# Kernel optimization log

Measured on AMD Instinct MI355X. Metric: run time of the kernel, lower is better.

Reference implementation:

```python
import jax, jax.numpy as jnp
import numpy as np

N, IN_DIM, OUT_DIM = 8192, 256, 128
NEG_BIG = -9e15


def setup_inputs() -> dict:
    key = jax.random.key(0)
    k_x, k_a, k_w, k_att = jax.random.split(key, 4)
    X = jax.random.normal(k_x, (N, IN_DIM), dtype=jnp.float32)
    A = jax.random.randint(k_a, (N, N), 0, 2).astype(jnp.float32)
    # nn.Linear(in_dim, out_dim, bias=False): weight [out_dim, in_dim]
    W = jax.random.normal(k_w, (OUT_DIM, IN_DIM), dtype=jnp.float32) / np.sqrt(IN_DIM)
    # nn.Linear(out_dim, 1, bias=False): weight [1, out_dim] -> store as [out_dim]
    a_w = jax.random.normal(k_att, (OUT_DIM,), dtype=jnp.float32) / np.sqrt(OUT_DIM)
    return {"X": X, "A": A, "W": W, "a_w": a_w}


def reference(X, A, W, a_w):
    Wh = X @ W.T                                  # [N, out_dim]
    e = jax.nn.relu(Wh) @ a_w                      # [N]  (a(relu(Wh)).squeeze(-1))
    # NOTE: faithful to source: e broadcasts over rows -> score[i, j] = e[j]
    scores = jnp.where(A > 0, e[None, :], NEG_BIG)  # [N, N]
    attention = jax.nn.softmax(scores, axis=1)      # [N, N]
    h_prime = attention @ Wh                        # [N, out_dim]
    return jax.nn.relu(h_prime)
```

## Files before the change

### kernel.cpp

```cpp
#include <hip/hip_runtime.h>

typedef float        f32x4  __attribute__((ext_vector_type(4)));
typedef __bf16       bf16x8 __attribute__((ext_vector_type(8)));
typedef unsigned int u32x4  __attribute__((ext_vector_type(4)));

#define NN   8192
#define IND  256
#define OUTD 128
#define NB   144
#define KSPLIT 8
#define KRANGE 1024
#define KCHUNK 128
#define BSTRIDE 136

__device__ __forceinline__ bf16x8 cvt2(f32x4 a, f32x4 b) {
  bf16x8 r;
  r[0]=(__bf16)a[0]; r[1]=(__bf16)a[1]; r[2]=(__bf16)a[2]; r[3]=(__bf16)a[3];
  r[4]=(__bf16)b[0]; r[5]=(__bf16)b[1]; r[6]=(__bf16)b[2]; r[7]=(__bf16)b[3];
  return r;
}

__global__ __launch_bounds__(128) void k1_wh_e(const float* __restrict__ X,
                                               const float* __restrict__ W,
                                               const float* __restrict__ aw,
                                               float* __restrict__ Wh,
                                               float* __restrict__ ev) {
  const int lane = threadIdx.x & 63;
  const int wave = threadIdx.x >> 6;
  const int nlo  = lane & 15;
  const int quad = lane >> 4;
  const int rowBase = blockIdx.x * 32 + wave * 16;

  const float* xp = X + (size_t)(rowBase + nlo) * IND + quad * 8;
  f32x4 acc[8];
#pragma unroll
  for (int nt = 0; nt < 8; ++nt) acc[nt] = f32x4{0.f, 0.f, 0.f, 0.f};

#pragma unroll
  for (int kb = 0; kb < IND; kb += 32) {
    f32x4 a0 = *(const f32x4*)(xp + kb);
    f32x4 a1 = *(const f32x4*)(xp + kb + 4);
    bf16x8 af = cvt2(a0, a1);
#pragma unroll
    for (int nt = 0; nt < 8; ++nt) {
      const float* wp = W + (size_t)(nt * 16 + nlo) * IND + kb + quad * 8;
      f32x4 b0 = *(const f32x4*)wp;
      f32x4 b1 = *(const f32x4*)(wp + 4);
      acc[nt] = __builtin_amdgcn_mfma_f32_16x16x32_bf16(af, cvt2(b0, b1), acc[nt], 0, 0, 0);
    }
  }
  float p0 = 0.f, p1 = 0.f, p2 = 0.f, p3 = 0.f;
#pragma unroll
  for (int nt = 0; nt < 8; ++nt) {
    const int col = nt * 16 + nlo;
    const float awc = aw[col];
    const int r0 = rowBase + quad * 4;
    float v0 = acc[nt][0], v1 = acc[nt][1], v2 = acc[nt][2], v3 = acc[nt][3];
    Wh[(size_t)(r0 + 0) * OUTD + col] = v0;
    Wh[(size_t)(r0 + 1) * OUTD + col] = v1;
    Wh[(size_t)(r0 + 2) * OUTD + col] = v2;
    Wh[(size_t)(r0 + 3) * OUTD + col] = v3;
    p0 += fmaxf(v0, 0.f) * awc;
    p1 += fmaxf(v1, 0.f) * awc;
    p2 += fmaxf(v2, 0.f) * awc;
    p3 += fmaxf(v3, 0.f) * awc;
  }
#pragma unroll
  for (int off = 8; off; off >>= 1) {
    p0 += __shfl_xor(p0, off, 64);
    p1 += __shfl_xor(p1, off, 64);
    p2 += __shfl_xor(p2, off, 64);
    p3 += __shfl_xor(p3, off, 64);
  }
  if (nlo == 0) {
    const int r0 = rowBase + quad * 4;
    ev[r0 + 0] = p0; ev[r0 + 1] = p1; ev[r0 + 2] = p2; ev[r0 + 3] = p3;
  }
}

__global__ __launch_bounds__(256) void k2_bt(const float* __restrict__ Wh,
                                             const float* __restrict__ ev,
                                             __bf16* __restrict__ Bt) {
  const int j = blockIdx.x * 256 + threadIdx.x;
  const float w = expf(ev[j]);
  const int n0 = blockIdx.y * 18;
#pragma unroll
  for (int i = 0; i < 18; ++i) {
    const int n = n0 + i;
    float v = 0.f;
    if (n < OUTD) v = w * Wh[(size_t)j * OUTD + n];
    else if (n == OUTD) v = w;
    Bt[(size_t)n * NN + j] = (__bf16)v;
  }
}

__global__ __launch_bounds__(256, 4) void k3_partial(const float* __restrict__ Adj,
                                                     const __bf16* __restrict__ Bt,
                                                     float* __restrict__ part) {
  __shared__ unsigned short bt[NB * BSTRIDE];
  const int tid  = threadIdx.x;
  const int lane = tid & 63;
  const int wave = tid >> 6;
  const int nlo  = lane & 15;
  const int quad = lane >> 4;
  const int rowW = blockIdx.x * 64 + wave * 16;
  const int k0   = blockIdx.y * KRANGE;

  const int brow = tid >> 4;
  const int bcol = (tid & 15) * 8;

  f32x4 acc[9];
#pragma unroll
  for (int nt = 0; nt < 9; ++nt) acc[nt] = f32x4{0.f, 0.f, 0.f, 0.f};

  const float* ap = Adj + (size_t)(rowW + nlo) * NN + quad * 8 + k0;

  for (int c = 0; c < KRANGE / KCHUNK; ++c) {
    const int kc = k0 + c * KCHUNK;
    u32x4 breg[9];
#pragma unroll
    for (int rr = 0; rr < 9; ++rr)
      breg[rr] = *(const u32x4*)(Bt + (size_t)(rr * 16 + brow) * NN + kc + bcol);
    f32x4 areg[8];
#pragma unroll
    for (int s = 0; s < 4; ++s) {
      areg[2 * s]     = __builtin_nontemporal_load((const f32x4*)(ap + c * KCHUNK + s * 32));
      areg[2 * s + 1] = __builtin_nontemporal_load((const f32x4*)(ap + c * KCHUNK + s * 32 + 4));
    }
#pragma unroll
    for (int rr = 0; rr < 9; ++rr)
      *(u32x4*)(bt + (rr * 16 + brow) * BSTRIDE + bcol) = breg[rr];
    __syncthreads();
#pragma unroll
    for (int s = 0; s < 4; ++s) {
      bf16x8 af = cvt2(areg[2 * s], areg[2 * s + 1]);
      const unsigned short* bp = bt + s * 32 + quad * 8;
#pragma unroll
      for (int nt = 0; nt < 9; ++nt) {
        bf16x8 bf = *(const bf16x8*)(bp + (nt * 16 + nlo) * BSTRIDE);
        acc[nt] = __builtin_amdgcn_mfma_f32_16x16x32_bf16(af, bf, acc[nt], 0, 0, 0);
      }
    }
    __syncthreads();
  }

  float* pbase = part + ((size_t)blockIdx.y * NN + rowW) * NB;
#pragma unroll
  for (int nt = 0; nt < 9; ++nt)
#pragma unroll
    for (int rg = 0; rg < 4; ++rg)
      pbase[(size_t)(quad * 4 + rg) * NB + nt * 16 + nlo] = acc[nt][rg];
}

__global__ __launch_bounds__(256) void k3_reduce(const float* __restrict__ part,
                                                 float* __restrict__ out) {
  const int col = threadIdx.x & 127;
  const int row = blockIdx.x * 2 + (threadIdx.x >> 7);
  float num = 0.f, den = 0.f;
#pragma unroll
  for (int s = 0; s < KSPLIT; ++s) {
    const size_t base = ((size_t)s * NN + row) * NB;
    num += part[base + col];
    den += part[base + 128];
  }
  out[(size_t)row * OUTD + col] = fmaxf(num / den, 0.f);
}

extern "C" void kernel_launch(void* const* d_in, const int* in_sizes, int n_in,
                              void* d_out, int out_size, void* d_ws, size_t ws_size,
                              hipStream_t stream) {
  const float* X  = (const float*)d_in[0];
  const float* A  = (const float*)d_in[1];
  const float* W  = (const float*)d_in[2];
  const float* aw = (const float*)d_in[3];
  float* out = (float*)d_out;

  char* ws = (char*)d_ws;
  float*  Wh   = (float*)ws;
  float*  ev   = (float*)(ws + 4194304);
  __bf16* Bt   = (__bf16*)(ws + 4227072);
  float*  part = (float*)(ws + 8388608);

  k1_wh_e<<<256, 128, 0, stream>>>(X, W, aw, Wh, ev);
  k2_bt<<<dim3(32, 8), 256, 0, stream>>>(Wh, ev, Bt);
  k3_partial<<<dim3(128, KSPLIT), 256, 0, stream>>>(A, Bt, part);
  k3_reduce<<<4096, 256, 0, stream>>>(part, out);
}
```

Before: 432.2 us.

## Fuse Bt construction into Wh kernel and read B operand directly from global

The first kernel now computes exp(e), scales Wh in registers and writes the transposed bf16 B matrix, including the denominator row and zero padding, directly. This removes the intermediate fp32 Wh/ev round trip and one kernel launch. The main attention kernel drops its LDS staging of B and the two barriers per chunk, loading B fragments straight from global memory and relying on L2/L1 reuse across blocks. The cost is possibly less coalesced B loads per wave and more cache traffic in the bandwidth-bound stage that streams A.

```diff
diff --git a/kernel.cpp b/kernel.cpp
--- a/kernel.cpp
+++ b/kernel.cpp
@@ -2,7 +2,7 @@
 
 typedef float        f32x4  __attribute__((ext_vector_type(4)));
 typedef __bf16       bf16x8 __attribute__((ext_vector_type(8)));
-typedef unsigned int u32x4  __attribute__((ext_vector_type(4)));
+typedef __bf16       bf16x4 __attribute__((ext_vector_type(4)));
 
 #define NN   8192
 #define IND  256
@@ -11,7 +11,6 @@
 #define KSPLIT 8
 #define KRANGE 1024
 #define KCHUNK 128
-#define BSTRIDE 136
 
 __device__ __forceinline__ bf16x8 cvt2(f32x4 a, f32x4 b) {
   bf16x8 r;
@@ -20,11 +19,10 @@
   return r;
 }
 
-__global__ __launch_bounds__(128) void k1_wh_e(const float* __restrict__ X,
-                                               const float* __restrict__ W,
-                                               const float* __restrict__ aw,
-                                               float* __restrict__ Wh,
-                                               float* __restrict__ ev) {
+__global__ __launch_bounds__(128) void k1_bt(const float* __restrict__ X,
+                                             const float* __restrict__ W,
+                                             const float* __restrict__ aw,
+                                             __bf16* __restrict__ Bt) {
   const int lane = threadIdx.x & 63;
   const int wave = threadIdx.x >> 6;
   const int nlo  = lane & 15;
@@ -49,21 +47,15 @@
       acc[nt] = __builtin_amdgcn_mfma_f32_16x16x32_bf16(af, cvt2(b0, b1), acc[nt], 0, 0, 0);
     }
   }
+
   float p0 = 0.f, p1 = 0.f, p2 = 0.f, p3 = 0.f;
 #pragma unroll
   for (int nt = 0; nt < 8; ++nt) {
-    const int col = nt * 16 + nlo;
-    const float awc = aw[col];
-    const int r0 = rowBase + quad * 4;
-    float v0 = acc[nt][0], v1 = acc[nt][1], v2 = acc[nt][2], v3 = acc[nt][3];
-    Wh[(size_t)(r0 + 0) * OUTD + col] = v0;
-    Wh[(size_t)(r0 + 1) * OUTD + col] = v1;
-    Wh[(size_t)(r0 + 2) * OUTD + col] = v2;
-    Wh[(size_t)(r0 + 3) * OUTD + col] = v3;
-    p0 += fmaxf(v0, 0.f) * awc;
-    p1 += fmaxf(v1, 0.f) * awc;
-    p2 += fmaxf(v2, 0.f) * awc;
-    p3 += fmaxf(v3, 0.f) * awc;
+    const float awc = aw[nt * 16 + nlo];
+    p0 += fmaxf(acc[nt][0], 0.f) * awc;
+    p1 += fmaxf(acc[nt][1], 0.f) * awc;
+    p2 += fmaxf(acc[nt][2], 0.f) * awc;
+    p3 += fmaxf(acc[nt][3], 0.f) * awc;
   }
 #pragma unroll
   for (int off = 8; off; off >>= 1) {
@@ -72,55 +64,53 @@
     p2 += __shfl_xor(p2, off, 64);
     p3 += __shfl_xor(p3, off, 64);
   }
+  const float w0 = expf(p0), w1 = expf(p1), w2 = expf(p2), w3 = expf(p3);
+  const int r0 = rowBase + quad * 4;
+
+#pragma unroll
+  for (int nt = 0; nt < 8; ++nt) {
+    bf16x4 o;
+    o[0] = (__bf16)(acc[nt][0] * w0);
+    o[1] = (__bf16)(acc[nt][1] * w1);
+    o[2] = (__bf16)(acc[nt][2] * w2);
+    o[3] = (__bf16)(acc[nt][3] * w3);
+    *(bf16x4*)(Bt + (size_t)(nt * 16 + nlo) * NN + r0) = o;
+  }
   if (nlo == 0) {
-    const int r0 = rowBase + quad * 4;
-    ev[r0 + 0] = p0; ev[r0 + 1] = p1; ev[r0 + 2] = p2; ev[r0 + 3] = p3;
+    bf16x4 ow;
+    ow[0] = (__bf16)w0; ow[1] = (__bf16)w1; ow[2] = (__bf16)w2; ow[3] = (__bf16)w3;
+    *(bf16x4*)(Bt + (size_t)OUTD * NN + r0) = ow;
   }
-}
-
-__global__ __launch_bounds__(256) void k2_bt(const float* __restrict__ Wh,
-                                             const float* __restrict__ ev,
-                                             __bf16* __restrict__ Bt) {
-  const int j = blockIdx.x * 256 + threadIdx.x;
-  const float w = expf(ev[j]);
-  const int n0 = blockIdx.y * 18;
-#pragma unroll
-  for (int i = 0; i < 18; ++i) {
-    const int n = n0 + i;
-    float v = 0.f;
-    if (n < OUTD) v = w * Wh[(size_t)j * OUTD + n];
-    else if (n == OUTD) v = w;
-    Bt[(size_t)n * NN + j] = (__bf16)v;
+  {
+    const int t = threadIdx.x;
+    if (t < 120) {
+      const int row = 129 + (t >> 3);
+      const int cg  = (t & 7) * 4;
+      bf16x4 z;
+      z[0] = (__bf16)0.f; z[1] = (__bf16)0.f; z[2] = (__bf16)0.f; z[3] = (__bf16)0.f;
+      *(bf16x4*)(Bt + (size_t)row * NN + blockIdx.x * 32 + cg) = z;
+    }
   }
 }
 
 __global__ __launch_bounds__(256, 4) void k3_partial(const float* __restrict__ Adj,
                                                      const __bf16* __restrict__ Bt,
                                                      float* __restrict__ part) {
-  __shared__ unsigned short bt[NB * BSTRIDE];
-  const int tid  = threadIdx.x;
-  const int lane = tid & 63;
-  const int wave = tid >> 6;
+  const int lane = threadIdx.x & 63;
+  const int wave = threadIdx.x >> 6;
   const int nlo  = lane & 15;
   const int quad = lane >> 4;
   const int rowW = blockIdx.x * 64 + wave * 16;
   const int k0   = blockIdx.y * KRANGE;
 
-  const int brow = tid >> 4;
-  const int bcol = (tid & 15) * 8;
-
   f32x4 acc[9];
 #pragma unroll
   for (int nt = 0; nt < 9; ++nt) acc[nt] = f32x4{0.f, 0.f, 0.f, 0.f};
 
-  const float* ap = Adj + (size_t)(rowW + nlo) * NN + quad * 8 + k0;
+  const float*  ap = Adj + (size_t)(rowW + nlo) * NN + quad * 8 + k0;
+  const __bf16* bp = Bt  + (size_t)nlo * NN + quad * 8 + k0;
 
   for (int c = 0; c < KRANGE / KCHUNK; ++c) {
-    const int kc = k0 + c * KCHUNK;
-    u32x4 breg[9];
-#pragma unroll
-    for (int rr = 0; rr < 9; ++rr)
-      breg[rr] = *(const u32x4*)(Bt + (size_t)(rr * 16 + brow) * NN + kc + bcol);
     f32x4 areg[8];
 #pragma unroll
     for (int s = 0; s < 4; ++s) {
@@ -128,20 +118,14 @@
       areg[2 * s + 1] = __builtin_nontemporal_load((const f32x4*)(ap + c * KCHUNK + s * 32 + 4));
     }
 #pragma unroll
-    for (int rr = 0; rr < 9; ++rr)
-      *(u32x4*)(bt + (rr * 16 + brow) * BSTRIDE + bcol) = breg[rr];
-    __syncthreads();
-#pragma unroll
     for (int s = 0; s < 4; ++s) {
       bf16x8 af = cvt2(areg[2 * s], areg[2 * s + 1]);
-      const unsigned short* bp = bt + s * 32 + quad * 8;
 #pragma unroll
       for (int nt = 0; nt < 9; ++nt) {
-        bf16x8 bf = *(const bf16x8*)(bp + (nt * 16 + nlo) * BSTRIDE);
+        bf16x8 bf = *(const bf16x8*)(bp + (size_t)(nt * 16) * NN + c * KCHUNK + s * 32);
         acc[nt] = __builtin_amdgcn_mfma_f32_16x16x32_bf16(af, bf, acc[nt], 0, 0, 0);
       }
     }
-    __syncthreads();
   }
 
   float* pbase = part + ((size_t)blockIdx.y * NN + rowW) * NB;
@@ -176,13 +160,10 @@
   float* out = (float*)d_out;
 
   char* ws = (char*)d_ws;
-  float*  Wh   = (float*)ws;
-  float*  ev   = (float*)(ws + 4194304);
-  __bf16* Bt   = (__bf16*)(ws + 4227072);
-  float*  part = (float*)(ws + 8388608);
+  __bf16* Bt   = (__bf16*)ws;
+  float*  part = (float*)(ws + 4194304);
 
-  k1_wh_e<<<256, 128, 0, stream>>>(X, W, aw, Wh, ev);
-  k2_bt<<<dim3(32, 8), 256, 0, stream>>>(Wh, ev, Bt);
+  k1_bt<<<256, 128, 0, stream>>>(X, W, aw, Bt);
   k3_partial<<<dim3(128, KSPLIT), 256, 0, stream>>>(A, Bt, part);
   k3_reduce<<<4096, 256, 0, stream>>>(part, out);
 }
```

Measured after the change: 500.5 us. +15.8%, slower.

## Register double-buffer adjacency/B loads in k3 and split-K the Wh projection

Applied to the files above, without the earlier changes.

The main aggregation kernel now prefetches the next chunk of adjacency rows and Bt tiles into a second register set while MFMAs run on the current chunk, so global memory latency overlaps with compute. Its occupancy hint drops from 4 to 2 blocks per CU to make room for the extra registers. The first kernel splits the 256-wide K dimension across four waves and reduces through shared memory, which doubles the grid and allows vectorized Wh stores. The denominator column of the partial output is now written only by lanes with nlo==0 instead of by 16 lanes holding padding.

```diff
diff --git a/kernel.cpp b/kernel.cpp
--- a/kernel.cpp
+++ b/kernel.cpp
@@ -2,6 +2,7 @@
 
 typedef float        f32x4  __attribute__((ext_vector_type(4)));
 typedef __bf16       bf16x8 __attribute__((ext_vector_type(8)));
+typedef __bf16       bf16x4 __attribute__((ext_vector_type(4)));
 typedef unsigned int u32x4  __attribute__((ext_vector_type(4)));
 
 #define NN   8192
@@ -20,62 +21,65 @@
   return r;
 }
 
-__global__ __launch_bounds__(128) void k1_wh_e(const float* __restrict__ X,
+__global__ __launch_bounds__(256) void k1_wh_e(const float* __restrict__ X,
                                                const float* __restrict__ W,
                                                const float* __restrict__ aw,
                                                float* __restrict__ Wh,
                                                float* __restrict__ ev) {
-  const int lane = threadIdx.x & 63;
-  const int wave = threadIdx.x >> 6;
+  __shared__ float red[4][16][128];
+  const int tid  = threadIdx.x;
+  const int lane = tid & 63;
+  const int wave = tid >> 6;
   const int nlo  = lane & 15;
   const int quad = lane >> 4;
-  const int rowBase = blockIdx.x * 32 + wave * 16;
-
-  const float* xp = X + (size_t)(rowBase + nlo) * IND + quad * 8;
+  const int rowBase = blockIdx.x * 16;
+
+  const float* xp = X + (size_t)(rowBase + nlo) * IND + wave * 64 + quad * 8;
   f32x4 acc[8];
 #pragma unroll
   for (int nt = 0; nt < 8; ++nt) acc[nt] = f32x4{0.f, 0.f, 0.f, 0.f};
 
 #pragma unroll
-  for (int kb = 0; kb < IND; kb += 32) {
+  for (int kb = 0; kb < 64; kb += 32) {
     f32x4 a0 = *(const f32x4*)(xp + kb);
     f32x4 a1 = *(const f32x4*)(xp + kb + 4);
     bf16x8 af = cvt2(a0, a1);
 #pragma unroll
     for (int nt = 0; nt < 8; ++nt) {
-      const float* wp = W + (size_t)(nt * 16 + nlo) * IND + kb + quad * 8;
+      const float* wp = W + (size_t)(nt * 16 + nlo) * IND + wave * 64 + kb + quad * 8;
       f32x4 b0 = *(const f32x4*)wp;
       f32x4 b1 = *(const f32x4*)(wp + 4);
       acc[nt] = __builtin_amdgcn_mfma_f32_16x16x32_bf16(af, cvt2(b0, b1), acc[nt], 0, 0, 0);
     }
   }
-  float p0 = 0.f, p1 = 0.f, p2 = 0.f, p3 = 0.f;
-#pragma unroll
-  for (int nt = 0; nt < 8; ++nt) {
-    const int col = nt * 16 + nlo;
-    const float awc = aw[col];
-    const int r0 = rowBase + quad * 4;
-    float v0 = acc[nt][0], v1 = acc[nt][1], v2 = acc[nt][2], v3 = acc[nt][3];
-    Wh[(size_t)(r0 + 0) * OUTD + col] = v0;
-    Wh[(size_t)(r0 + 1) * OUTD + col] = v1;
-    Wh[(size_t)(r0 + 2) * OUTD + col] = v2;
-    Wh[(size_t)(r0 + 3) * OUTD + col] = v3;
-    p0 += fmaxf(v0, 0.f) * awc;
-    p1 += fmaxf(v1, 0.f) * awc;
-    p2 += fmaxf(v2, 0.f) * awc;
-    p3 += fmaxf(v3, 0.f) * awc;
-  }
-#pragma unroll
-  for (int off = 8; off; off >>= 1) {
-    p0 += __shfl_xor(p0, off, 64);
-    p1 += __shfl_xor(p1, off, 64);
-    p2 += __shfl_xor(p2, off, 64);
-    p3 += __shfl_xor(p3, off, 64);
-  }
-  if (nlo == 0) {
-    const int r0 = rowBase + quad * 4;
-    ev[r0 + 0] = p0; ev[r0 + 1] = p1; ev[r0 + 2] = p2; ev[r0 + 3] = p3;
-  }
+#pragma unroll
+  for (int nt = 0; nt < 8; ++nt)
+#pragma unroll
+    for (int rg = 0; rg < 4; ++rg)
+      red[wave][quad * 4 + rg][nt * 16 + nlo] = acc[nt][rg];
+  __syncthreads();
+
+  const int r  = tid >> 4;
+  const int c0 = (tid & 15) * 8;
+  f32x4 vlo = *(const f32x4*)&red[0][r][c0];
+  f32x4 vhi = *(const f32x4*)&red[0][r][c0 + 4];
+#pragma unroll
+  for (int w = 1; w < 4; ++w) {
+    vlo += *(const f32x4*)&red[w][r][c0];
+    vhi += *(const f32x4*)&red[w][r][c0 + 4];
+  }
+  *(f32x4*)(Wh + (size_t)(rowBase + r) * OUTD + c0)     = vlo;
+  *(f32x4*)(Wh + (size_t)(rowBase + r) * OUTD + c0 + 4) = vhi;
+
+  float pa = 0.f;
+#pragma unroll
+  for (int j = 0; j < 4; ++j) {
+    pa += fmaxf(vlo[j], 0.f) * aw[c0 + j];
+    pa += fmaxf(vhi[j], 0.f) * aw[c0 + 4 + j];
+  }
+#pragma unroll
+  for (int off = 8; off; off >>= 1) pa += __shfl_xor(pa, off, 64);
+  if ((tid & 15) == 0) ev[rowBase + r] = pa;
 }
 
 __global__ __launch_bounds__(256) void k2_bt(const float* __restrict__ Wh,
@@ -94,7 +98,7 @@
   }
 }
 
-__global__ __launch_bounds__(256, 4) void k3_partial(const float* __restrict__ Adj,
+__global__ __launch_bounds__(256, 2) void k3_partial(const float* __restrict__ Adj,
                                                      const __bf16* __restrict__ Bt,
                                                      float* __restrict__ part) {
   __shared__ unsigned short bt[NB * BSTRIDE];
@@ -113,27 +117,43 @@
 #pragma unroll
   for (int nt = 0; nt < 9; ++nt) acc[nt] = f32x4{0.f, 0.f, 0.f, 0.f};
 
-  const float* ap = Adj + (size_t)(rowW + nlo) * NN + quad * 8 + k0;
+  const float*  ap = Adj + (size_t)(rowW + nlo) * NN + quad * 8 + k0;
+  const __bf16* bq = Bt + (size_t)brow * NN + k0 + bcol;
+
+  u32x4 bregA[9];
+  f32x4 aregA[8];
+#pragma unroll
+  for (int rr = 0; rr < 9; ++rr)
+    bregA[rr] = *(const u32x4*)(bq + (size_t)(rr * 16) * NN);
+#pragma unroll
+  for (int s = 0; s < 4; ++s) {
+    aregA[2 * s]     = __builtin_nontemporal_load((const f32x4*)(ap + s * 32));
+    aregA[2 * s + 1] = __builtin_nontemporal_load((const f32x4*)(ap + s * 32 + 4));
+  }
 
   for (int c = 0; c < KRANGE / KCHUNK; ++c) {
-    const int kc = k0 + c * KCHUNK;
-    u32x4 breg[9];
 #pragma unroll
     for (int rr = 0; rr < 9; ++rr)
-      breg[rr] = *(const u32x4*)(Bt + (size_t)(rr * 16 + brow) * NN + kc + bcol);
-    f32x4 areg[8];
+      *(u32x4*)(bt + (rr * 16 + brow) * BSTRIDE + bcol) = bregA[rr];
+    __syncthreads();
+
+    u32x4 bregB[9];
+    f32x4 aregB[8];
+    if (c < KRANGE / KCHUNK - 1) {
+      const int kc1 = (c + 1) * KCHUNK;
+#pragma unroll
+      for (int rr = 0; rr < 9; ++rr)
+        bregB[rr] = *(const u32x4*)(bq + (size_t)(rr * 16) * NN + kc1);
+#pragma unroll
+      for (int s = 0; s < 4; ++s) {
+        aregB[2 * s]     = __builtin_nontemporal_load((const f32x4*)(ap + kc1 + s * 32));
+        aregB[2 * s + 1] = __builtin_nontemporal_load((const f32x4*)(ap + kc1 + s * 32 + 4));
+      }
+    }
+
 #pragma unroll
     for (int s = 0; s < 4; ++s) {
-      areg[2 * s]     = __builtin_nontemporal_load((const f32x4*)(ap + c * KCHUNK + s * 32));
-      areg[2 * s + 1] = __builtin_nontemporal_load((const f32x4*)(ap + c * KCHUNK + s * 32 + 4));
-    }
-#pragma unroll
-    for (int rr = 0; rr < 9; ++rr)
-      *(u32x4*)(bt + (rr * 16 + brow) * BSTRIDE + bcol) = breg[rr];
-    __syncthreads();
-#pragma unroll
-    for (int s = 0; s < 4; ++s) {
-      bf16x8 af = cvt2(areg[2 * s], areg[2 * s + 1]);
+      bf16x8 af = cvt2(aregA[2 * s], aregA[2 * s + 1]);
       const unsigned short* bp = bt + s * 32 + quad * 8;
 #pragma unroll
       for (int nt = 0; nt < 9; ++nt) {
@@ -142,14 +162,26 @@
       }
     }
     __syncthreads();
+
+    if (c < KRANGE / KCHUNK - 1) {
+#pragma unroll
+      for (int rr = 0; rr < 9; ++rr) bregA[rr] = bregB[rr];
+#pragma unroll
+      for (int s = 0; s < 8; ++s) aregA[s] = aregB[s];
+    }
   }
 
   float* pbase = part + ((size_t)blockIdx.y * NN + rowW) * NB;
 #pragma unroll
-  for (int nt = 0; nt < 9; ++nt)
+  for (int nt = 0; nt < 8; ++nt)
 #pragma unroll
     for (int rg = 0; rg < 4; ++rg)
       pbase[(size_t)(quad * 4 + rg) * NB + nt * 16 + nlo] = acc[nt][rg];
+  if (nlo == 0) {
+#pragma unroll
+    for (int rg = 0; rg < 4; ++rg)
+      pbase[(size_t)(quad * 4 + rg) * NB + 128] = acc[8][rg];
+  }
 }
 
 __global__ __launch_bounds__(256) void k3_reduce(const float* __restrict__ part,
@@ -181,7 +213,7 @@
   __bf16* Bt   = (__bf16*)(ws + 4227072);
   float*  part = (float*)(ws + 8388608);
 
-  k1_wh_e<<<256, 128, 0, stream>>>(X, W, aw, Wh, ev);
+  k1_wh_e<<<512, 256, 0, stream>>>(X, W, aw, Wh, ev);
   k2_bt<<<dim3(32, 8), 256, 0, stream>>>(Wh, ev, Bt);
   k3_partial<<<dim3(128, KSPLIT), 256, 0, stream>>>(A, Bt, part);
   k3_reduce<<<4096, 256, 0, stream>>>(part, out);
```

New measurement: 415.1 us. 4.0% less time.
